# Optimization experiments

Measured on AMD Instinct MI355X. Metric: run time of the kernel, lower is better.

Reference implementation:

```python
import jax, jax.numpy as jnp
import numpy as np

N_NODES = 50000
N_EDGES = 800000
IN_C = 128
HID_C = 128
OUT_C = 128
ATT_H = 64
EPS_COS = 1e-8
EPS_EUD = 1e-6


def _cos_sim(a, b):
    # torch.cosine_similarity(dim=1): dot / max(|a|*|b|, eps)
    num = jnp.sum(a * b, axis=1)
    den = jnp.maximum(jnp.linalg.norm(a, axis=1) * jnp.linalg.norm(b, axis=1), EPS_COS)
    return num / den


def _eud(a, b):
    # nn.PairwiseDistance(p=2): ||a - b + eps||_2
    d = a - b + EPS_EUD
    return jnp.sqrt(jnp.sum(d * d, axis=1))


def _sage(x, row, col, ew, Wl, bl, Wr):
    # SAGEConv with edge weights: mean_j(ew_ij * x_j) @ Wl + bl + x_i @ Wr
    msg = x[col] * ew[:, None]                               # [E, C]
    agg = jax.ops.segment_sum(msg, row, num_segments=N_NODES)  # [N, C]
    deg = jax.ops.segment_sum(jnp.ones_like(ew), row, num_segments=N_NODES)
    agg = agg / jnp.maximum(deg, 1.0)[:, None]
    return agg @ Wl + bl + x @ Wr


def setup_inputs() -> dict:
    key = jax.random.key(0)
    ks = jax.random.split(key, 12)
    s = 0.05
    return {
        "x": jax.random.normal(ks[0], (N_NODES, IN_C), jnp.float32),
        "row": jax.random.randint(ks[1], (N_EDGES,), 0, N_NODES),
        "col": jax.random.randint(ks[2], (N_EDGES,), 0, N_NODES),
        "Wl0": jax.random.normal(ks[3], (IN_C, HID_C), jnp.float32) * s,
        "bl0": jax.random.normal(ks[4], (HID_C,), jnp.float32) * s,
        "Wr0": jax.random.normal(ks[5], (IN_C, HID_C), jnp.float32) * s,
        "Wl1": jax.random.normal(ks[6], (HID_C, OUT_C), jnp.float32) * s,
        "bl1": jax.random.normal(ks[7], (OUT_C,), jnp.float32) * s,
        "Wr1": jax.random.normal(ks[8], (HID_C, OUT_C), jnp.float32) * s,
        "attW1": jax.random.normal(ks[9], (HID_C, ATT_H), jnp.float32) * s,
        "attb1": jax.random.normal(ks[10], (ATT_H,), jnp.float32) * s,
        "attW2": jax.random.normal(ks[11], (ATT_H, 1), jnp.float32) * s,
    }


def reference(x, row, col, Wl0, bl0, Wr0, Wl1, bl1, Wr1, attW1, attb1, attW2):
    xs, xd = x[row], x[col]
    # cosine branch (dropout is a no-op in eval mode)
    e_cos = _cos_sim(xs, xd)
    x3 = jax.nn.relu(_sage(x, row, col, e_cos, Wl0, bl0, Wr0))   # [N, HID]
    e_cos2 = _cos_sim(x3[row], x3[col])
    x1 = _sage(x3, row, col, e_cos2, Wl1, bl1, Wr1)              # [N, OUT]
    # euclidean branch
    e_eud = _eud(xs, xd)
    x4 = jax.nn.relu(_sage(x, row, col, e_eud, Wl0, bl0, Wr0))   # [N, HID]
    e_eud2 = _eud(x4[row], x4[col])
    x2 = _sage(x4, row, col, e_eud2, Wl1, bl1, Wr1)              # [N, OUT]
    # attention pooling over the 4 branch embeddings
    z = jnp.stack([x1, x2, x3, x4], axis=1)                      # [N, 4, C]
    w = jnp.tanh(z @ attW1 + attb1) @ attW2                      # [N, 4, 1]
    beta = jax.nn.softmax(w, axis=1)
    emb = jnp.sum(beta * z, axis=1)                              # [N, C]
    return (emb, x3, x4)
```

## Files before the change

### kernel.cpp

```cpp
#include <hip/hip_runtime.h>

#define NN 50000
#define NE 800000
#define C 128
#define CAP 64
#define CAPSH 6

typedef __attribute__((ext_vector_type(8))) short short8_t;
typedef __attribute__((ext_vector_type(4))) float f32x4;
typedef __attribute__((ext_vector_type(2))) float f32x2;
typedef __attribute__((ext_vector_type(2))) _Float16 half2_t;
typedef __attribute__((ext_vector_type(8))) _Float16 half8_t;

__device__ __forceinline__ unsigned short f2h_u(float f) {
    _Float16 h = (_Float16)f;
    union { _Float16 h; unsigned short u; } v; v.h = h; return v.u;
}

__device__ __forceinline__ float fdot2(half2_t a, half2_t b, float c) {
#if __has_builtin(__builtin_amdgcn_fdot2)
    return __builtin_amdgcn_fdot2(a, b, c, false);
#else
    return c + (float)a.x * (float)b.x + (float)a.y * (float)b.y;
#endif
}

__device__ __forceinline__ float rsq_fast(float x) {
#if __has_builtin(__builtin_amdgcn_rsqf)
    return __builtin_amdgcn_rsqf(x);
#else
    float r; asm volatile("v_rsq_f32 %0, %1" : "=v"(r) : "v"(x)); return r;
#endif
}
__device__ __forceinline__ float sqrt_fast(float x) {
#if __has_builtin(__builtin_amdgcn_sqrtf)
    return __builtin_amdgcn_sqrtf(x);
#else
    float r; asm volatile("v_sqrt_f32 %0, %1" : "=v"(r) : "v"(x)); return r;
#endif
}

template <int CTRL>
__device__ __forceinline__ float dpp_add(float x) {
    int y = __builtin_amdgcn_update_dpp(0, __float_as_int(x), CTRL, 0xF, 0xF, false);
    return x + __int_as_float(y);
}
__device__ __forceinline__ float qred16(float x) {
    x = dpp_add<0xB1>(x);
    x = dpp_add<0x4E>(x);
    x = dpp_add<0x141>(x);
    x = dpp_add<0x140>(x);
    return x;
}

#define BUCK_NB ((NE + 255) / 256)
#define CAST_NB (NN / 4)
#define PREP_NB ((65536 + 8192) / 256)
__global__ void cast_prep(const float* __restrict__ x, unsigned short* __restrict__ xh,
                          float2* __restrict__ st1,
                          const float* __restrict__ Wl0, const float* __restrict__ Wr0,
                          const float* __restrict__ Wl1, const float* __restrict__ Wr1,
                          const float* __restrict__ aW1,
                          unsigned short* __restrict__ Bt, unsigned short* __restrict__ BtA,
                          const int* __restrict__ row, const int* __restrict__ col,
                          int* __restrict__ cnt, int* __restrict__ colv) {
    if (blockIdx.x < BUCK_NB) {
        int e = blockIdx.x * 256 + threadIdx.x;
        if (e < NE) {
            int r = row[e];
            int p = atomicAdd(&cnt[r], 1);
            if (p < CAP) colv[(r << CAPSH) + p] = col[e];
        }
    } else if (blockIdx.x < BUCK_NB + CAST_NB) {
        int node = (blockIdx.x - BUCK_NB) * 4 + (threadIdx.x >> 6);
        int lane = threadIdx.x & 63;
        float2 v = *(const float2*)(x + (size_t)node * C + lane * 2);
        half2_t h; h.x = (_Float16)v.x; h.y = (_Float16)v.y;
        *(half2_t*)(xh + (size_t)node * C + lane * 2) = h;
        float sq = v.x * v.x + v.y * v.y;
        float sm = v.x + v.y;
#pragma unroll
        for (int off = 32; off > 0; off >>= 1) {
            sq += __shfl_xor(sq, off, 64);
            sm += __shfl_xor(sm, off, 64);
        }
        if (lane == 0) st1[node] = make_float2(sq, sm);
    } else {
        int id = (blockIdx.x - BUCK_NB - CAST_NB) * 256 + threadIdx.x;
        if (id < 65536) {
            int layer = id >> 15;
            int c = (id >> 14) & 1;
            int n = (id >> 7) & 127;
            int kk = id & 127;
            const float* W = layer == 0 ? (c == 0 ? Wl0 : Wr0) : (c == 0 ? Wl1 : Wr1);
            Bt[id] = f2h_u(W[kk * 128 + n]);
        } else {
            int a = id - 65536;
            int cl = a >> 7, k = a & 127;
            BtA[a] = f2h_u(aW1[k * 64 + cl]);
        }
    }
}

__global__ void stats2h(const unsigned short* __restrict__ x34h, float4* __restrict__ st2) {
    int node = blockIdx.x * 4 + (threadIdx.x >> 6);
    int lane = threadIdx.x & 63;
    const unsigned short* base = x34h + (size_t)node * 256 + lane * 2;
    half2_t a = *(const half2_t*)(base);
    half2_t b = *(const half2_t*)(base + 128);
    float q3 = fdot2(a, a, 0.f);
    float q4 = fdot2(b, b, 0.f);
    float m4 = (float)b.x + (float)b.y;
#pragma unroll
    for (int off = 32; off > 0; off >>= 1) {
        q3 += __shfl_xor(q3, off, 64);
        q4 += __shfl_xor(q4, off, 64);
        m4 += __shfl_xor(m4, off, 64);
    }
    if (lane == 0) st2[node] = make_float4(q3, q4, m4, 0.f);
}

__global__ __launch_bounds__(256) void fused_l1(
    const unsigned short* __restrict__ xh, const int* __restrict__ colv,
    const int* __restrict__ cnts, const float2* __restrict__ st1,
    unsigned short* __restrict__ aggc, unsigned short* __restrict__ agge) {
    int node = blockIdx.x * 4 + (threadIdx.x >> 6);
    int lane = threadIdx.x & 63;
    int q = lane >> 4, lq = lane & 15;
    int cnt = cnts[node];
    int beg = node << CAPSH, end = beg + cnt;
    half8_t xr = *(const half8_t*)(xh + (size_t)node * C + lq * 8);
    float2 sr = st1[node];
    float n2r = sr.x, s1r = sr.y;
    f32x2 ac[4] = {};
    f32x2 ae[4] = {};
    for (int p = beg; p < end; p += 4) {
        int pe = p + q;
        bool valid = pe < end;
        int pc = valid ? pe : (end - 1);
        int c0 = colv[pc];
        half8_t u = *(const half8_t*)(xh + (size_t)c0 * C + lq * 8);
        float2 t0 = st1[c0];
        float d = 0.f;
#pragma unroll
        for (int i = 0; i < 4; ++i) {
            half2_t a; a.x = xr[2 * i]; a.y = xr[2 * i + 1];
            half2_t b; b.x = u[2 * i]; b.y = u[2 * i + 1];
            d = fdot2(a, b, d);
        }
        d = qred16(d);
        float wc0 = d * rsq_fast(fmaxf(n2r * t0.x, 1e-16f));
        float qq = n2r + t0.x - 2.f * d + 2e-6f * (s1r - t0.y) + 1.28e-10f;
        float we0 = sqrt_fast(fmaxf(qq, 0.f));
        if (!valid) { wc0 = 0.f; we0 = 0.f; }
        f32x2 wcv; wcv.x = wc0; wcv.y = wc0;
        f32x2 wev; wev.x = we0; wev.y = we0;
#pragma unroll
        for (int i = 0; i < 4; ++i) {
            f32x2 uf; uf.x = (float)u[2 * i]; uf.y = (float)u[2 * i + 1];
            ac[i] += wcv * uf;
            ae[i] += wev * uf;
        }
    }
#pragma unroll
    for (int i = 0; i < 4; ++i) {
#pragma unroll
        for (int k = 0; k < 2; ++k) {
            float vc = ac[i][k], ve = ae[i][k];
            vc += __shfl_xor(vc, 16, 64);
            vc += __shfl_xor(vc, 32, 64);
            ve += __shfl_xor(ve, 16, 64);
            ve += __shfl_xor(ve, 32, 64);
            ac[i][k] = vc; ae[i][k] = ve;
        }
    }
    if (q == 0) {
        float inv = 1.f / fmaxf((float)cnt, 1.f);
        half8_t hc, he;
#pragma unroll
        for (int i = 0; i < 4; ++i) {
            hc[2 * i]     = (_Float16)(ac[i].x * inv);
            hc[2 * i + 1] = (_Float16)(ac[i].y * inv);
            he[2 * i]     = (_Float16)(ae[i].x * inv);
            he[2 * i + 1] = (_Float16)(ae[i].y * inv);
        }
        *(half8_t*)(aggc + (size_t)node * C + lq * 8) = hc;
        *(half8_t*)(agge + (size_t)node * C + lq * 8) = he;
    }
}

__global__ __launch_bounds__(256) void fused_l2(
    const unsigned short* __restrict__ x34h,
    const int* __restrict__ colv, const int* __restrict__ cnts,
    const float4* __restrict__ st2,
    unsigned short* __restrict__ agg1, unsigned short* __restrict__ agg2) {
    int node = blockIdx.x * 4 + (threadIdx.x >> 6);
    int lane = threadIdx.x & 63;
    int q = lane >> 4, lq = lane & 15;
    int cnt = cnts[node];
    int beg = node << CAPSH, end = beg + cnt;
    const unsigned short* nb = x34h + (size_t)node * 256 + lq * 8;
    half8_t x3r = *(const half8_t*)(nb);
    half8_t x4r = *(const half8_t*)(nb + 128);
    float4 sr = st2[node];
    f32x2 a1[4] = {};
    f32x2 a2[4] = {};
    for (int p = beg; p < end; p += 4) {
        int pe = p + q;
        bool valid = pe < end;
        int pc = valid ? pe : (end - 1);
        int c0 = colv[pc];
        const unsigned short* cb = x34h + (size_t)c0 * 256 + lq * 8;
        half8_t u = *(const half8_t*)(cb);
        half8_t v = *(const half8_t*)(cb + 128);
        float4 t0 = st2[c0];
        float d3 = 0.f, d4 = 0.f;
#pragma unroll
        for (int i = 0; i < 4; ++i) {
            half2_t a; a.x = x3r[2 * i]; a.y = x3r[2 * i + 1];
            half2_t b; b.x = u[2 * i]; b.y = u[2 * i + 1];
            d3 = fdot2(a, b, d3);
            half2_t e; e.x = x4r[2 * i]; e.y = x4r[2 * i + 1];
            half2_t f; f.x = v[2 * i]; f.y = v[2 * i + 1];
            d4 = fdot2(e, f, d4);
        }
        d3 = qred16(d3);
        d4 = qred16(d4);
        float wc0 = d3 * rsq_fast(fmaxf(sr.x * t0.x, 1e-16f));
        float qq = sr.y + t0.y - 2.f * d4 + 2e-6f * (sr.z - t0.z) + 1.28e-10f;
        float we0 = sqrt_fast(fmaxf(qq, 0.f));
        if (!valid) { wc0 = 0.f; we0 = 0.f; }
        f32x2 wcv; wcv.x = wc0; wcv.y = wc0;
        f32x2 wev; wev.x = we0; wev.y = we0;
#pragma unroll
        for (int i = 0; i < 4; ++i) {
            f32x2 uf; uf.x = (float)u[2 * i]; uf.y = (float)u[2 * i + 1];
            f32x2 vf; vf.x = (float)v[2 * i]; vf.y = (float)v[2 * i + 1];
            a1[i] += wcv * uf;
            a2[i] += wev * vf;
        }
    }
#pragma unroll
    for (int i = 0; i < 4; ++i) {
#pragma unroll
        for (int k = 0; k < 2; ++k) {
            float v1 = a1[i][k], v2 = a2[i][k];
            v1 += __shfl_xor(v1, 16, 64);
            v1 += __shfl_xor(v1, 32, 64);
            v2 += __shfl_xor(v2, 16, 64);
            v2 += __shfl_xor(v2, 32, 64);
            a1[i][k] = v1; a2[i][k] = v2;
        }
    }
    if (q == 0) {
        float inv = 1.f / fmaxf((float)cnt, 1.f);
        half8_t h1, h2;
#pragma unroll
        for (int i = 0; i < 4; ++i) {
            h1[2 * i]     = (_Float16)(a1[i].x * inv);
            h1[2 * i + 1] = (_Float16)(a1[i].y * inv);
            h2[2 * i]     = (_Float16)(a2[i].x * inv);
            h2[2 * i + 1] = (_Float16)(a2[i].y * inv);
        }
        *(half8_t*)(agg1 + (size_t)node * C + lq * 8) = h1;
        *(half8_t*)(agg2 + (size_t)node * C + lq * 8) = h2;
    }
}

__global__ __launch_bounds__(256) void gemm_dual(
    const unsigned short* __restrict__ A0a, const unsigned short* __restrict__ A0b,
    const unsigned short* __restrict__ A1a, const unsigned short* __restrict__ A1b,
    int a1stride,
    const unsigned short* __restrict__ Bt, const float* __restrict__ bias,
    float* __restrict__ Couta, float* __restrict__ Coutb,
    unsigned short* __restrict__ Chfa, unsigned short* __restrict__ Chfb,
    int chfstride, int relu) {
    __shared__ __align__(16) unsigned short sA[128 * 136];
    __shared__ __align__(16) unsigned short sB[128 * 136];
    const int br = blockIdx.y;
    const unsigned short* A0 = br ? A0b : A0a;
    const unsigned short* A1 = br ? A1b : A1a;
    float* Cout = br ? Coutb : Couta;
    unsigned short* Chf = br ? Chfb : Chfa;
    const int tx = threadIdx.x;
    const int l = tx & 63;
    const int wv = tx >> 6;
    const int wm = wv >> 1, wn = wv & 1;
    const int lr = l & 15;
    const int lq = l >> 4;
    const int n0 = blockIdx.x * 128;

    f32x4 acc[4][4] = {};
    for (int c = 0; c < 2; ++c) {
        const unsigned short* Ac = (c == 0) ? A0 : A1;
        const size_t strideA = (c == 0) ? 128 : a1stride;
#pragma unroll
        for (int it = 0; it < 8; ++it) {
            int idx = it * 256 + tx;
            int r = idx >> 4, s = idx & 15;
            int n = n0 + r; n = n < NN ? n : NN - 1;
            *(short8_t*)(sA + r * 136 + s * 8) = *(const short8_t*)(Ac + (size_t)n * strideA + s * 8);
            *(short8_t*)(sB + r * 136 + s * 8) = *(const short8_t*)(Bt + c * 16384 + idx * 8);
        }
        __syncthreads();
#pragma unroll
        for (int ks = 0; ks < 4; ++ks) {
            half8_t af[4], bfr[4];
#pragma unroll
            for (int t = 0; t < 4; ++t) {
                af[t]  = *(const half8_t*)(sA + (wm * 64 + t * 16 + lr) * 136 + ks * 32 + lq * 8);
                bfr[t] = *(const half8_t*)(sB + (wn * 64 + t * 16 + lr) * 136 + ks * 32 + lq * 8);
            }
#pragma unroll
            for (int mt = 0; mt < 4; ++mt)
#pragma unroll
                for (int nt = 0; nt < 4; ++nt)
                    acc[mt][nt] = __builtin_amdgcn_mfma_f32_16x16x32_f16(af[mt], bfr[nt], acc[mt][nt], 0, 0, 0);
        }
        __syncthreads();
    }
#pragma unroll
    for (int mt = 0; mt < 4; ++mt) {
        int rbase = wm * 64 + mt * 16 + lq * 4;
#pragma unroll
        for (int nt = 0; nt < 4; ++nt) {
            int col = wn * 64 + nt * 16 + lr;
            float bv = bias[col];
#pragma unroll
            for (int rg = 0; rg < 4; ++rg) {
                int n = n0 + rbase + rg;
                if (n < NN) {
                    float y = acc[mt][nt][rg] + bv;
                    if (relu) y = fmaxf(y, 0.f);
                    if (Cout) Cout[(size_t)n * 128 + col] = y;
                    Chf[(size_t)n * chfstride + col] = f2h_u(y);
                }
            }
        }
    }
}

__global__ __launch_bounds__(256) void att_fused(
    const unsigned short* __restrict__ x12h, const unsigned short* __restrict__ x34h,
    const unsigned short* __restrict__ BtA, const float* __restrict__ b1,
    const float* __restrict__ W2, float* __restrict__ emb) {
    __shared__ __align__(16) unsigned short sA[128 * 136];
    __shared__ __align__(16) unsigned short sB[64 * 136];
    __shared__ float sW[32][4];
    const int tx = threadIdx.x;
    const int n0 = blockIdx.x * 32;
#pragma unroll
    for (int it = 0; it < 8; ++it) {
        int idx = it * 256 + tx;
        int r = idx >> 4, s = idx & 15;
        int node = n0 + (r >> 2); node = node < NN ? node : NN - 1;
        int b = r & 3;
        const unsigned short* src = (b < 2 ? x12h : x34h) + (size_t)node * 256 + (b & 1) * 128 + s * 8;
        *(short8_t*)(sA + r * 136 + s * 8) = *(const short8_t*)(src);
    }
#pragma unroll
    for (int it = 0; it < 4; ++it) {
        int idx = it * 256 + tx;
        int r = idx >> 4, s = idx & 15;
        *(short8_t*)(sB + r * 136 + s * 8) = *(const short8_t*)(BtA + idx * 8);
    }
    __syncthreads();
    const int w = tx >> 6, lane = tx & 63, lr = lane & 15, lq = lane >> 4;
    f32x4 acc[2][4] = {};
#pragma unroll
    for (int ks = 0; ks < 4; ++ks) {
        half8_t af[2], bfr[4];
#pragma unroll
        for (int mt = 0; mt < 2; ++mt)
            af[mt] = *(const half8_t*)(sA + (w * 32 + mt * 16 + lr) * 136 + ks * 32 + lq * 8);
#pragma unroll
        for (int nt = 0; nt < 4; ++nt)
            bfr[nt] = *(const half8_t*)(sB + (nt * 16 + lr) * 136 + ks * 32 + lq * 8);
#pragma unroll
        for (int mt = 0; mt < 2; ++mt)
#pragma unroll
            for (int nt = 0; nt < 4; ++nt)
                acc[mt][nt] = __builtin_amdgcn_mfma_f32_16x16x32_f16(af[mt], bfr[nt], acc[mt][nt], 0, 0, 0);
    }
#pragma unroll
    for (int mt = 0; mt < 2; ++mt) {
        float part[4] = {0.f, 0.f, 0.f, 0.f};
#pragma unroll
        for (int nt = 0; nt < 4; ++nt) {
            int col = nt * 16 + lr;
            float bb = b1[col], w2 = W2[col];
#pragma unroll
            for (int rg = 0; rg < 4; ++rg) {
                float h = acc[mt][nt][rg] + bb;
                float cl = fminf(fmaxf(h, -15.f), 15.f);
                float e2 = __expf(2.f * cl);
                part[rg] += (e2 - 1.f) / (e2 + 1.f) * w2;
            }
        }
#pragma unroll
        for (int rg = 0; rg < 4; ++rg)
#pragma unroll
            for (int off = 1; off < 16; off <<= 1)
                part[rg] += __shfl_xor(part[rg], off, 64);
        if (lr == 0) {
#pragma unroll
            for (int rg = 0; rg < 4; ++rg) {
                int r = w * 32 + mt * 16 + lq * 4 + rg;
                sW[r >> 2][r & 3] = part[rg];
            }
        }
    }
    __syncthreads();
    int ln = tx >> 3;
    int node = n0 + ln;
    if (node < NN) {
        int ch0 = (tx & 7) * 16;
        float w0 = sW[ln][0], w1 = sW[ln][1], w2 = sW[ln][2], w3 = sW[ln][3];
        float m = fmaxf(fmaxf(w0, w1), fmaxf(w2, w3));
        float e0 = __expf(w0 - m), e1 = __expf(w1 - m), e2 = __expf(w2 - m), e3 = __expf(w3 - m);
        float inv = 1.f / (e0 + e1 + e2 + e3);
        float bt[4] = {e0 * inv, e1 * inv, e2 * inv, e3 * inv};
        float o[16];
#pragma unroll
        for (int i = 0; i < 16; ++i) o[i] = 0.f;
#pragma unroll
        for (int b = 0; b < 4; ++b) {
            int rowoff = (ln * 4 + b) * 136 + ch0;
            half8_t h0 = *(const half8_t*)(sA + rowoff);
            half8_t h1 = *(const half8_t*)(sA + rowoff + 8);
            float bb = bt[b];
#pragma unroll
            for (int i = 0; i < 8; ++i) {
                o[i]     += bb * (float)h0[i];
                o[8 + i] += bb * (float)h1[i];
            }
        }
        float* dst = emb + (size_t)node * 128 + ch0;
#pragma unroll
        for (int i = 0; i < 4; ++i) {
            float4 v4; v4.x = o[4 * i]; v4.y = o[4 * i + 1]; v4.z = o[4 * i + 2]; v4.w = o[4 * i + 3];
            *(float4*)(dst + 4 * i) = v4;
        }
    }
}

extern "C" void kernel_launch(void* const* d_in, const int* in_sizes, int n_in,
                              void* d_out, int out_size, void* d_ws, size_t ws_size,
                              hipStream_t stream) {
    const float* x   = (const float*)d_in[0];
    const int* row   = (const int*)d_in[1];
    const int* col   = (const int*)d_in[2];
    const float* Wl0 = (const float*)d_in[3];
    const float* bl0 = (const float*)d_in[4];
    const float* Wr0 = (const float*)d_in[5];
    const float* Wl1 = (const float*)d_in[6];
    const float* bl1 = (const float*)d_in[7];
    const float* Wr1 = (const float*)d_in[8];
    const float* aW1 = (const float*)d_in[9];
    const float* ab1 = (const float*)d_in[10];
    const float* aW2 = (const float*)d_in[11];

    float* out = (float*)d_out;
    float* emb = out;
    float* x3  = out + (size_t)NN * C;
    float* x4  = out + 2 * (size_t)NN * C;

    char* ws = (char*)d_ws;
    size_t off = 0;
    auto alloc = [&](size_t bytes) -> void* {
        void* p = ws + off;
        off += (bytes + 255) & ~(size_t)255;
        return p;
    };
    int* cnt     = (int*)alloc((size_t)NN * 4);
    int* colv    = (int*)alloc((size_t)NN * CAP * 4);
    float2* st1  = (float2*)alloc((size_t)NN * 8);
    float4* st2  = (float4*)alloc((size_t)NN * 16);
    unsigned short* xh    = (unsigned short*)alloc((size_t)NN * C * 2);
    unsigned short* aggch = (unsigned short*)alloc((size_t)NN * C * 2);
    unsigned short* aggeh = (unsigned short*)alloc((size_t)NN * C * 2);
    unsigned short* x34h  = (unsigned short*)alloc((size_t)NN * 256 * 2);
    unsigned short* x12h  = (unsigned short*)alloc((size_t)NN * 256 * 2);
    unsigned short* Bt    = (unsigned short*)alloc((size_t)65536 * 2);
    unsigned short* BtA   = (unsigned short*)alloc((size_t)8192 * 2);

    hipMemsetAsync(cnt, 0, (size_t)NN * 4, stream);

    cast_prep<<<BUCK_NB + CAST_NB + PREP_NB, 256, 0, stream>>>(
        x, xh, st1, Wl0, Wr0, Wl1, Wr1, aW1, Bt, BtA, row, col, cnt, colv);

    fused_l1<<<NN / 4, 256, 0, stream>>>(xh, colv, cnt, st1, aggch, aggeh);

    const int GB = (NN + 127) / 128;
    gemm_dual<<<dim3(GB, 2), 256, 0, stream>>>(
        aggch, aggeh, xh, xh, 128, Bt, bl0,
        x3, x4, x34h, x34h + 128, 256, 1);

    stats2h<<<NN / 4, 256, 0, stream>>>(x34h, st2);
    fused_l2<<<NN / 4, 256, 0, stream>>>(x34h, colv, cnt, st2, aggch, aggeh);

    gemm_dual<<<dim3(GB, 2), 256, 0, stream>>>(
        aggch, aggeh, x34h, x34h + 128, 256, Bt + 32768, bl1,
        nullptr, nullptr, x12h, x12h + 128, 256, 0);

    att_fused<<<(NN + 31) / 32, 256, 0, stream>>>(x12h, x34h, BtA, ab1, aW2, emb);
}
```

Baseline: 351.8 us.

## Fuse layer-2 node stats into GEMM epilogue and shuffle-broadcast neighbor indices

Result: faster. 330.9 us (-5.9%).

```diff
diff --git a/kernel.cpp b/kernel.cpp
--- a/kernel.cpp
+++ b/kernel.cpp
@@ -102,24 +102,6 @@
     }
 }
 
-__global__ void stats2h(const unsigned short* __restrict__ x34h, float4* __restrict__ st2) {
-    int node = blockIdx.x * 4 + (threadIdx.x >> 6);
-    int lane = threadIdx.x & 63;
-    const unsigned short* base = x34h + (size_t)node * 256 + lane * 2;
-    half2_t a = *(const half2_t*)(base);
-    half2_t b = *(const half2_t*)(base + 128);
-    float q3 = fdot2(a, a, 0.f);
-    float q4 = fdot2(b, b, 0.f);
-    float m4 = (float)b.x + (float)b.y;
-#pragma unroll
-    for (int off = 32; off > 0; off >>= 1) {
-        q3 += __shfl_xor(q3, off, 64);
-        q4 += __shfl_xor(q4, off, 64);
-        m4 += __shfl_xor(m4, off, 64);
-    }
-    if (lane == 0) st2[node] = make_float4(q3, q4, m4, 0.f);
-}
-
 __global__ __launch_bounds__(256) void fused_l1(
     const unsigned short* __restrict__ xh, const int* __restrict__ colv,
     const int* __restrict__ cnts, const float2* __restrict__ st1,
@@ -127,18 +109,19 @@
     int node = blockIdx.x * 4 + (threadIdx.x >> 6);
     int lane = threadIdx.x & 63;
     int q = lane >> 4, lq = lane & 15;
-    int cnt = cnts[node];
-    int beg = node << CAPSH, end = beg + cnt;
+    int cnt_raw = cnts[node];
+    int cnt = cnt_raw < CAP ? cnt_raw : CAP;
+    int cv = colv[(node << CAPSH) + lane];
     half8_t xr = *(const half8_t*)(xh + (size_t)node * C + lq * 8);
     float2 sr = st1[node];
     float n2r = sr.x, s1r = sr.y;
     f32x2 ac[4] = {};
     f32x2 ae[4] = {};
-    for (int p = beg; p < end; p += 4) {
-        int pe = p + q;
-        bool valid = pe < end;
-        int pc = valid ? pe : (end - 1);
-        int c0 = colv[pc];
+    for (int p = 0; p < cnt; p += 4) {
+        int ei = p + q;
+        bool valid = ei < cnt;
+        int src = valid ? ei : (cnt - 1);
+        int c0 = __shfl(cv, src, 64);
         half8_t u = *(const half8_t*)(xh + (size_t)c0 * C + lq * 8);
         float2 t0 = st1[c0];
         float d = 0.f;
@@ -175,7 +158,7 @@
         }
     }
     if (q == 0) {
-        float inv = 1.f / fmaxf((float)cnt, 1.f);
+        float inv = 1.f / fmaxf((float)cnt_raw, 1.f);
         half8_t hc, he;
 #pragma unroll
         for (int i = 0; i < 4; ++i) {
@@ -197,19 +180,20 @@
     int node = blockIdx.x * 4 + (threadIdx.x >> 6);
     int lane = threadIdx.x & 63;
     int q = lane >> 4, lq = lane & 15;
-    int cnt = cnts[node];
-    int beg = node << CAPSH, end = beg + cnt;
+    int cnt_raw = cnts[node];
+    int cnt = cnt_raw < CAP ? cnt_raw : CAP;
+    int cv = colv[(node << CAPSH) + lane];
     const unsigned short* nb = x34h + (size_t)node * 256 + lq * 8;
     half8_t x3r = *(const half8_t*)(nb);
     half8_t x4r = *(const half8_t*)(nb + 128);
     float4 sr = st2[node];
     f32x2 a1[4] = {};
     f32x2 a2[4] = {};
-    for (int p = beg; p < end; p += 4) {
-        int pe = p + q;
-        bool valid = pe < end;
-        int pc = valid ? pe : (end - 1);
-        int c0 = colv[pc];
+    for (int p = 0; p < cnt; p += 4) {
+        int ei = p + q;
+        bool valid = ei < cnt;
+        int src = valid ? ei : (cnt - 1);
+        int c0 = __shfl(cv, src, 64);
         const unsigned short* cb = x34h + (size_t)c0 * 256 + lq * 8;
         half8_t u = *(const half8_t*)(cb);
         half8_t v = *(const half8_t*)(cb + 128);
@@ -253,7 +237,7 @@
         }
     }
     if (q == 0) {
-        float inv = 1.f / fmaxf((float)cnt, 1.f);
+        float inv = 1.f / fmaxf((float)cnt_raw, 1.f);
         half8_t h1, h2;
 #pragma unroll
         for (int i = 0; i < 4; ++i) {
@@ -274,7 +258,7 @@
     const unsigned short* __restrict__ Bt, const float* __restrict__ bias,
     float* __restrict__ Couta, float* __restrict__ Coutb,
     unsigned short* __restrict__ Chfa, unsigned short* __restrict__ Chfb,
-    int chfstride, int relu) {
+    int chfstride, int relu, float* __restrict__ st2f) {
     __shared__ __align__(16) unsigned short sA[128 * 136];
     __shared__ __align__(16) unsigned short sB[128 * 136];
     const int br = blockIdx.y;
@@ -319,21 +303,45 @@
         }
         __syncthreads();
     }
+    float* sP2 = (float*)sA;
+    float* sP1 = sP2 + 256;
 #pragma unroll
     for (int mt = 0; mt < 4; ++mt) {
         int rbase = wm * 64 + mt * 16 + lq * 4;
 #pragma unroll
-        for (int nt = 0; nt < 4; ++nt) {
-            int col = wn * 64 + nt * 16 + lr;
-            float bv = bias[col];
-#pragma unroll
-            for (int rg = 0; rg < 4; ++rg) {
-                int n = n0 + rbase + rg;
+        for (int rg = 0; rg < 4; ++rg) {
+            int n = n0 + rbase + rg;
+            float s2 = 0.f, s1 = 0.f;
+#pragma unroll
+            for (int nt = 0; nt < 4; ++nt) {
+                int col = wn * 64 + nt * 16 + lr;
+                float y = acc[mt][nt][rg] + bias[col];
+                if (relu) y = fmaxf(y, 0.f);
+                s2 += y * y; s1 += y;
                 if (n < NN) {
-                    float y = acc[mt][nt][rg] + bv;
-                    if (relu) y = fmaxf(y, 0.f);
                     if (Cout) Cout[(size_t)n * 128 + col] = y;
                     Chf[(size_t)n * chfstride + col] = f2h_u(y);
+                }
+            }
+            if (st2f) {
+                s2 = qred16(s2);
+                s1 = qred16(s1);
+                int rloc = rbase + rg;
+                if (lr == 0) { sP2[rloc * 2 + wn] = s2; sP1[rloc * 2 + wn] = s1; }
+            }
+        }
+    }
+    if (st2f) {
+        __syncthreads();
+        if (tx < 128) {
+            int n = n0 + tx;
+            if (n < NN) {
+                float q2 = sP2[tx * 2] + sP2[tx * 2 + 1];
+                if (br == 0) {
+                    st2f[(size_t)n * 4 + 0] = q2;
+                } else {
+                    st2f[(size_t)n * 4 + 1] = q2;
+                    st2f[(size_t)n * 4 + 2] = sP1[tx * 2] + sP1[tx * 2 + 1];
                 }
             }
         }
@@ -494,14 +502,13 @@
     const int GB = (NN + 127) / 128;
     gemm_dual<<<dim3(GB, 2), 256, 0, stream>>>(
         aggch, aggeh, xh, xh, 128, Bt, bl0,
-        x3, x4, x34h, x34h + 128, 256, 1);
-
-    stats2h<<<NN / 4, 256, 0, stream>>>(x34h, st2);
+        x3, x4, x34h, x34h + 128, 256, 1, (float*)st2);
+
     fused_l2<<<NN / 4, 256, 0, stream>>>(x34h, colv, cnt, st2, aggch, aggeh);
 
     gemm_dual<<<dim3(GB, 2), 256, 0, stream>>>(
         aggch, aggeh, x34h, x34h + 128, 256, Bt + 32768, bl1,
-        nullptr, nullptr, x12h, x12h + 128, 256, 0);
+        nullptr, nullptr, x12h, x12h + 128, 256, 0, nullptr);
 
     att_fused<<<(NN + 31) / 32, 256, 0, stream>>>(x12h, x34h, BtA, ab1, aW2, emb);
 }
```
